# Kernel optimization log

Hardware: AMD Instinct MI355X
Metric: run time of the kernel (lower is better)

## Reference

```python
import jax, jax.numpy as jnp
import numpy as np

NUM_HEADS = 16


def setup_inputs() -> dict:
    key = jax.random.key(0)
    ks = jax.random.split(key, 6)
    B, N, L, C = 2, 1024, 4096, 1024
    x_obj = jax.random.normal(ks[0], (B, N, C), dtype=jnp.float32)
    x_ctx = jax.random.normal(ks[1], (B, L, C), dtype=jnp.float32)
    s = 1.0 / np.sqrt(C)
    Wq = jax.random.normal(ks[2], (C, C), dtype=jnp.float32) * s
    Wkv = jax.random.normal(ks[3], (C, 2 * C), dtype=jnp.float32) * s
    Wproj = jax.random.normal(ks[4], (C, C), dtype=jnp.float32) * s
    bproj = jax.random.normal(ks[5], (C,), dtype=jnp.float32) * 0.01
    return {"x_obj": x_obj, "x_ctx": x_ctx, "Wq": Wq, "Wkv": Wkv,
            "Wproj": Wproj, "bproj": bproj}


def _split_heads(t, H):
    # [B, T, C] -> [B, H, T, d]
    B, T, C = t.shape
    return t.reshape(B, T, H, C // H).transpose(0, 2, 1, 3)


def reference(x_obj, x_ctx, Wq, Wkv, Wproj, bproj):
    B, N, C = x_obj.shape
    H = NUM_HEADS
    d = C // H
    scale = d ** -0.5

    q = _split_heads(x_obj @ Wq, H)                      # [B,H,N,d]

    kv_o = x_obj @ Wkv                                   # [B,N,2C] -> (2,H,d) split
    k_obj = _split_heads(kv_o[..., :C], H)               # [B,H,N,d]
    v_obj = _split_heads(kv_o[..., C:], H)

    kv_c = x_ctx @ Wkv                                   # [B,L,2C]
    k_ctx = _split_heads(kv_c[..., :C], H)               # [B,H,L,d]
    v_ctx = _split_heads(kv_c[..., C:], H)

    k = jnp.concatenate([k_obj, k_ctx], axis=2)          # [B,H,N+L,d]
    v = jnp.concatenate([v_obj, v_ctx], axis=2)

    attn = jnp.einsum('bhnd,bhmd->bhnm', q, k) * scale   # [B,H,N,N+L]
    attn = jax.nn.softmax(attn, axis=-1)
    out = jnp.einsum('bhnm,bhmd->bhnd', attn, v)         # [B,H,N,d]
    out = out.transpose(0, 2, 1, 3).reshape(B, N, C)
    return out @ Wproj + bproj
```

## Files before the change

kernel.cpp:

```cpp
#include <hip/hip_runtime.h>
#include <stdint.h>

typedef unsigned short u16;
typedef unsigned int   u32;
typedef __attribute__((ext_vector_type(8))) short bf16x8;
typedef __attribute__((ext_vector_type(4))) float f32x4;

__device__ __forceinline__ u16 f2bf(float f) {
    union { float f; u32 u; } v; v.f = f;
    return (u16)((v.u + 0x7FFFu + ((v.u >> 16) & 1u)) >> 16);
}
__device__ __forceinline__ float bf2f(u16 h) {
    union { u32 u; float f; } v; v.u = ((u32)h) << 16; return v.f;
}
__device__ __forceinline__ u32 fbits(float f) {
    union { float f; u32 u; } v; v.f = f; return v.u;
}

__device__ __forceinline__ void async16(const u16* g, u16* l) {
    typedef __attribute__((address_space(1))) const u32 gq;
    typedef __attribute__((address_space(3))) u32 lq;
    __builtin_amdgcn_global_load_lds((gq*)g, (lq*)l, 16, 0, 0);
}

__global__ void cvt_all_k(const float* __restrict__ xo, const float* __restrict__ xc,
                          u16* __restrict__ Xc,
                          const float* __restrict__ Wq, const float* __restrict__ Wkv,
                          const float* __restrict__ Wp,
                          u16* __restrict__ Wqt, u16* __restrict__ Wkt,
                          u16* __restrict__ Wpt)
{
    __shared__ __align__(16) u16 Ts[64][72];
    int id = blockIdx.x, t = threadIdx.x;
    if (id < 10240) {
        int row = id, cid = t * 4;
        int b = row >= 5120, s = row - b * 5120;
        const float* src = (s < 1024)
            ? xo + ((size_t)(b * 1024 + s)) * 1024 + cid
            : xc + ((size_t)(b * 4096 + s - 1024)) * 1024 + cid;
        float4 f = *(const float4*)src;
        union { u16 a[4]; uint2 v; } p;
        p.a[0]=f2bf(f.x); p.a[1]=f2bf(f.y); p.a[2]=f2bf(f.z); p.a[3]=f2bf(f.w);
        *(uint2*)(Xc + (size_t)row * 1024 + cid) = p.v;
        return;
    }
    int wid = id - 10240;
    const float* W; u16* Wt; int N, tile;
    if (wid < 256)      { W = Wq;  Wt = Wqt; N = 1024; tile = wid; }
    else if (wid < 768) { W = Wkv; Wt = Wkt; N = 2048; tile = wid - 256; }
    else                { W = Wp;  Wt = Wpt; N = 1024; tile = wid - 768; }
    int nt = N >> 6;
    int n0 = (tile % nt) * 64, k0 = (tile / nt) * 64;
    int lr = t >> 2, lc = (t & 3) * 16;
    const float* src = W + (size_t)(k0 + lr) * N + n0 + lc;
    union { u16 a[8]; uint4 v; } p0, p1;
    float4 f0 = *(const float4*)(src),      f1 = *(const float4*)(src + 4);
    float4 f2 = *(const float4*)(src + 8),  f3 = *(const float4*)(src + 12);
    p0.a[0]=f2bf(f0.x); p0.a[1]=f2bf(f0.y); p0.a[2]=f2bf(f0.z); p0.a[3]=f2bf(f0.w);
    p0.a[4]=f2bf(f1.x); p0.a[5]=f2bf(f1.y); p0.a[6]=f2bf(f1.z); p0.a[7]=f2bf(f1.w);
    p1.a[0]=f2bf(f2.x); p1.a[1]=f2bf(f2.y); p1.a[2]=f2bf(f2.z); p1.a[3]=f2bf(f2.w);
    p1.a[4]=f2bf(f3.x); p1.a[5]=f2bf(f3.y); p1.a[6]=f2bf(f3.z); p1.a[7]=f2bf(f3.w);
    *(uint4*)&Ts[lr][lc]     = p0.v;
    *(uint4*)&Ts[lr][lc + 8] = p1.v;
    __syncthreads();
    union { u16 a[8]; uint4 v; } q0, q1;
#pragma unroll
    for (int j = 0; j < 8; ++j) q0.a[j] = Ts[lc + j][lr];
#pragma unroll
    for (int j = 0; j < 8; ++j) q1.a[j] = Ts[lc + 8 + j][lr];
    u16* dst = Wt + (size_t)(n0 + lr) * 1024 + k0 + lc;
    *(uint4*)dst       = q0.v;
    *(uint4*)(dst + 8) = q1.v;
}

__global__ __launch_bounds__(256, 2)
void gemm_qkv(const u16* __restrict__ A, const u16* __restrict__ Wqt,
              const u16* __restrict__ Wkt, u16* __restrict__ q,
              u16* __restrict__ Kh, u16* __restrict__ Vh)
{
    __shared__ __align__(16) u16 smem[17408];
    u16* As = smem;
    u16* Bs = smem + 4096;

    const int t = threadIdx.x, w = t >> 6;
    const int lane = t & 63, quad = lane >> 4, l16 = lane & 15;
    const int id = blockIdx.x;
    const bool qm = id >= 1280;
    int m0, n0; const u16* Bt;
    if (qm) { int t2 = id - 1280; m0 = (t2 >> 3) * 128; n0 = (t2 & 7) * 128; Bt = Wqt; }
    else    { m0 = (id >> 4) * 128; n0 = (id & 15) * 128; Bt = Wkt; }
    const int wr = (w >> 1) * 64, wc = (w & 1) * 64;

    const int sr0 = w * 32 + (lane >> 2), sr1 = sr0 + 16;
    const int cg  = (lane & 3) ^ ((lane >> 4) & 3);
    u16* abase = As + w * 1024;
    u16* bbase = Bs + w * 1024;

    const u16 *ar0, *ar1;
    {
        int g0 = m0 + sr0, g1 = m0 + sr1;
        if (qm) {
            ar0 = A + ((size_t)(g0 >> 10) * 5120 + (g0 & 1023)) * 1024;
            ar1 = A + ((size_t)(g1 >> 10) * 5120 + (g1 & 1023)) * 1024;
        } else {
            ar0 = A + (size_t)g0 * 1024;
            ar1 = A + (size_t)g1 * 1024;
        }
        ar0 += cg * 8; ar1 += cg * 8;
    }
    const u16* br0 = Bt + (size_t)(n0 + sr0) * 1024 + cg * 8;
    const u16* br1 = Bt + (size_t)(n0 + sr1) * 1024 + cg * 8;

    f32x4 acc[4][4] = {};
    const int sel = (quad ^ (l16 >> 2)) * 8;

    for (int k0 = 0; k0 < 1024; k0 += 32) {
        async16(ar0 + k0, abase);
        async16(ar1 + k0, abase + 512);
        async16(br0 + k0, bbase);
        async16(br1 + k0, bbase + 512);
        __syncthreads();

        bf16x8 av[4], bv[4];
#pragma unroll
        for (int i = 0; i < 4; ++i)
            av[i] = *(const bf16x8*)&As[(wr + i * 16 + l16) * 32 + sel];
#pragma unroll
        for (int j = 0; j < 4; ++j)
            bv[j] = *(const bf16x8*)&Bs[(wc + j * 16 + l16) * 32 + sel];
#pragma unroll
        for (int i = 0; i < 4; ++i)
#pragma unroll
            for (int j = 0; j < 4; ++j)
                acc[i][j] = __builtin_amdgcn_mfma_f32_16x16x32_bf16(av[i], bv[j], acc[i][j], 0, 0, 0);
        __syncthreads();
    }

    if (qm) {
        const float SC = 0.180336880f;
#pragma unroll
        for (int j = 0; j < 4; ++j) {
            int col = n0 + wc + j * 16 + l16;
#pragma unroll
            for (int i = 0; i < 4; ++i) {
                int rowb = m0 + wr + i * 16 + quad * 4;
#pragma unroll
                for (int r = 0; r < 4; ++r)
                    q[(size_t)(rowb + r) * 1024 + col] = f2bf(acc[i][j][r] * SC);
            }
        }
        return;
    }
    int b = m0 >= 5120;
    int keyb = m0 - b * 5120;
    if (n0 < 1024) {
#pragma unroll
        for (int j = 0; j < 4; ++j) {
            int col = n0 + wc + j * 16 + l16;
#pragma unroll
            for (int i = 0; i < 4; ++i) {
                int rowb = m0 + wr + i * 16 + quad * 4;
                int key = rowb - b * 5120;
                int bh = b * 16 + (col >> 6), d = col & 63;
                u16* dst = Kh + ((size_t)bh * 5120 + key) * 64 + d;
#pragma unroll
                for (int r = 0; r < 4; ++r) dst[r * 64] = f2bf(acc[i][j][r]);
            }
        }
    } else {
        u16* T = smem;
#pragma unroll
        for (int j = 0; j < 4; ++j) {
            int d2 = wc + j * 16 + l16;
#pragma unroll
            for (int i = 0; i < 4; ++i) {
                int kl = wr + i * 16 + quad * 4;
                union { u16 a[4]; uint2 v; } pk;
#pragma unroll
                for (int r = 0; r < 4; ++r) pk.a[r] = f2bf(acc[i][j][r]);
                *(uint2*)&T[d2 * 136 + kl] = pk.v;
            }
        }
        __syncthreads();
        int hb = (n0 - 1024) >> 6;
#pragma unroll
        for (int p = 0; p < 8; ++p) {
            int idx = p * 256 + t;
            int d2 = idx >> 4, k0c = (idx & 15) * 8;
            uint4 vv = *(const uint4*)&T[d2 * 136 + k0c];
            int bh = b * 16 + hb + (d2 >> 6), d = d2 & 63;
            *(uint4*)(Vh + ((size_t)bh * 64 + d) * 5120 + keyb + k0c) = vv;
        }
    }
}

__global__ __launch_bounds__(256, 2)
void gemm_proj(const u16* __restrict__ A, const u16* __restrict__ Bt,
               const float* __restrict__ bias, float* __restrict__ Cf)
{
    __shared__ __align__(16) u16 As[128 * 32];
    __shared__ __align__(16) u16 Bs[64 * 32];

    const int t = threadIdx.x, w = t >> 6;
    const int lane = t & 63, quad = lane >> 4, l16 = lane & 15;
    const int m0 = blockIdx.y * 128, n0 = blockIdx.x * 64;
    const int wr = w * 32;

    const int sr0 = w * 32 + (lane >> 2), sr1 = sr0 + 16;
    const int cg  = (lane & 3) ^ ((lane >> 4) & 3);
    u16* abase = As + w * 1024;
    u16* bbase = Bs + w * 512;

    const u16* ar0 = A + (size_t)(m0 + sr0) * 1024 + cg * 8;
    const u16* ar1 = A + (size_t)(m0 + sr1) * 1024 + cg * 8;
    const u16* br0 = Bt + (size_t)(n0 + w * 16 + (lane >> 2)) * 1024 + cg * 8;

    f32x4 acc[2][4] = {};
    const int sel = (quad ^ (l16 >> 2)) * 8;

    for (int k0 = 0; k0 < 1024; k0 += 32) {
        async16(ar0 + k0, abase);
        async16(ar1 + k0, abase + 512);
        async16(br0 + k0, bbase);
        __syncthreads();

        bf16x8 av[2], bv[4];
#pragma unroll
        for (int i = 0; i < 2; ++i)
            av[i] = *(const bf16x8*)&As[(wr + i * 16 + l16) * 32 + sel];
#pragma unroll
        for (int j = 0; j < 4; ++j)
            bv[j] = *(const bf16x8*)&Bs[(j * 16 + l16) * 32 + sel];
#pragma unroll
        for (int i = 0; i < 2; ++i)
#pragma unroll
            for (int j = 0; j < 4; ++j)
                acc[i][j] = __builtin_amdgcn_mfma_f32_16x16x32_bf16(av[i], bv[j], acc[i][j], 0, 0, 0);
        __syncthreads();
    }

#pragma unroll
    for (int j = 0; j < 4; ++j) {
        int col = n0 + j * 16 + l16;
        float bvl = bias[col];
#pragma unroll
        for (int i = 0; i < 2; ++i) {
            int rowb = m0 + wr + i * 16 + quad * 4;
#pragma unroll
            for (int r = 0; r < 4; ++r)
                Cf[(size_t)(rowb + r) * 1024 + col] = acc[i][j][r] + bvl;
        }
    }
}

__global__ __launch_bounds__(256, 4)
void attn_k(const u16* __restrict__ Q, const u16* __restrict__ Kh,
            const u16* __restrict__ Vh, u16* __restrict__ Op,
            float* __restrict__ Lp)
{
    __shared__ __align__(16) u16 Ks[4096];
    __shared__ __align__(16) u16 Vt[4096];
    __shared__ __align__(16) u16 Ps[8192];

    const int tid  = threadIdx.x;
    const int wave = tid >> 6, lane = tid & 63;
    const int quad = lane >> 4, l16 = lane & 15;
    const int bx = blockIdx.x;
    const int part = bx & 3, qt = (bx >> 2) & 7, h = (bx >> 5) & 15, b = bx >> 9;
    const int bh = b * 16 + h;

    const int qrow0 = b * 1024 + qt * 128 + wave * 32;
    const u16* qbase = Q + (size_t)qrow0 * 1024 + h * 64;

    bf16x8 aq[2][2];
#pragma unroll
    for (int rt = 0; rt < 2; ++rt) {
        aq[rt][0] = *(const bf16x8*)(qbase + (size_t)(rt * 16 + l16) * 1024 +      quad * 8);
        aq[rt][1] = *(const bf16x8*)(qbase + (size_t)(rt * 16 + l16) * 1024 + 32 + quad * 8);
    }

    union { u32 u[4]; bf16x8 v; } onesf;
#pragma unroll
    for (int i = 0; i < 4; ++i) onesf.u[i] = 0x3F803F80u;

    f32x4 o[2][4] = {};
    f32x4 lacc[2] = {};

    const u16* kbase = Kh + (size_t)bh * 5120 * 64;
    const u16* vbase = Vh + (size_t)bh * 64 * 5120;
    const int srow = tid >> 2;
    const int scg  = (tid & 3) * 2;
    const int m7   = srow & 7;
    const int l7   = l16 & 7;
    u16* kdst0 = Ks + srow * 64 + ((scg ^ m7) * 8);
    u16* kdst1 = Ks + srow * 64 + (((scg + 1) ^ m7) * 8);
    u16* vdst0 = Vt + srow * 64 + ((scg ^ m7) * 8);
    u16* vdst1 = Vt + srow * 64 + (((scg + 1) ^ m7) * 8);
    u16* psw   = Ps + wave * 2048;
    const int m_beg = part * 1280;

    for (int c = 0; c < 20; ++c) {
        const int m0 = m_beg + c * 64;
        {
            const u16* ks = kbase + (size_t)(m0 + srow) * 64 + scg * 8;
            *(uint4*)kdst0 = *(const uint4*)(ks);
            *(uint4*)kdst1 = *(const uint4*)(ks + 8);
        }
        {
            const u16* vs = vbase + (size_t)srow * 5120 + m0 + (tid & 3) * 4;
            uint2 g0 = *(const uint2*)(vs);
            uint2 g1 = *(const uint2*)(vs + 16);
            uint2 g2 = *(const uint2*)(vs + 32);
            uint2 g3 = *(const uint2*)(vs + 48);
            uint4 o0, o1;
            o0.x = __builtin_amdgcn_perm(g1.x, g0.x, 0x05040100u);
            o0.y = __builtin_amdgcn_perm(g3.x, g2.x, 0x05040100u);
            o0.z = __builtin_amdgcn_perm(g1.x, g0.x, 0x07060302u);
            o0.w = __builtin_amdgcn_perm(g3.x, g2.x, 0x07060302u);
            o1.x = __builtin_amdgcn_perm(g1.y, g0.y, 0x05040100u);
            o1.y = __builtin_amdgcn_perm(g3.y, g2.y, 0x05040100u);
            o1.z = __builtin_amdgcn_perm(g1.y, g0.y, 0x07060302u);
            o1.w = __builtin_amdgcn_perm(g3.y, g2.y, 0x07060302u);
            *(uint4*)vdst0 = o0;
            *(uint4*)vdst1 = o1;
        }
        __syncthreads();

        f32x4 s[2][4] = {};
#pragma unroll
        for (int nt = 0; nt < 4; ++nt) {
            const u16* krow = Ks + (nt * 16 + l16) * 64;
            bf16x8 kb0 = *(const bf16x8*)(krow + ((quad     ^ l7) * 8));
            bf16x8 kb1 = *(const bf16x8*)(krow + (((4+quad) ^ l7) * 8));
#pragma unroll
            for (int rt = 0; rt < 2; ++rt) {
                s[rt][nt] = __builtin_amdgcn_mfma_f32_16x16x32_bf16(aq[rt][0], kb0, s[rt][nt], 0, 0, 0);
                s[rt][nt] = __builtin_amdgcn_mfma_f32_16x16x32_bf16(aq[rt][1], kb1, s[rt][nt], 0, 0, 0);
            }
        }

#pragma unroll
        for (int rt = 0; rt < 2; ++rt)
#pragma unroll
            for (int r = 0; r < 4; ++r) {
                float e0 = exp2f(s[rt][0][r]);
                float e1 = exp2f(s[rt][1][r]);
                float e2 = exp2f(s[rt][2][r]);
                float e3 = exp2f(s[rt][3][r]);
                uint2 pw;
                pw.x = __builtin_amdgcn_perm(fbits(e1), fbits(e0), 0x07060302u);
                pw.y = __builtin_amdgcn_perm(fbits(e3), fbits(e2), 0x07060302u);
                int qr = quad * 4 + r;
                *(uint2*)(psw + (rt * 16 + qr) * 64 +
                          (((l16 >> 1) ^ (qr & 7)) * 8) + (l16 & 1) * 4) = pw;
            }

        asm volatile("s_waitcnt lgkmcnt(0)" ::: "memory");

        bf16x8 pf[2][2];
#pragma unroll
        for (int rt = 0; rt < 2; ++rt) {
            const u16* prow = psw + (rt * 16 + l16) * 64;
            pf[rt][0] = *(const bf16x8*)(prow + ((quad     ^ l7) * 8));
            pf[rt][1] = *(const bf16x8*)(prow + (((4+quad) ^ l7) * 8));
        }

#pragma unroll
        for (int rt = 0; rt < 2; ++rt) {
            lacc[rt] = __builtin_amdgcn_mfma_f32_16x16x32_bf16(pf[rt][0], onesf.v, lacc[rt], 0, 0, 0);
            lacc[rt] = __builtin_amdgcn_mfma_f32_16x16x32_bf16(pf[rt][1], onesf.v, lacc[rt], 0, 0, 0);
        }

#pragma unroll
        for (int dt = 0; dt < 4; ++dt) {
            const u16* vrow = Vt + (dt * 16 + l16) * 64;
            bf16x8 v0 = *(const bf16x8*)(vrow + ((quad     ^ l7) * 8));
            bf16x8 v1 = *(const bf16x8*)(vrow + (((4+quad) ^ l7) * 8));
#pragma unroll
            for (int rt = 0; rt < 2; ++rt) {
                o[rt][dt] = __builtin_amdgcn_mfma_f32_16x16x32_bf16(pf[rt][0], v0, o[rt][dt], 0, 0, 0);
                o[rt][dt] = __builtin_amdgcn_mfma_f32_16x16x32_bf16(pf[rt][1], v1, o[rt][dt], 0, 0, 0);
            }
        }
        __syncthreads();
    }

    const int Rb = bh * 1024 + qt * 128 + wave * 32;
    u16* obase = Op + ((size_t)part << 21);
#pragma unroll
    for (int rt = 0; rt < 2; ++rt)
#pragma unroll
        for (int dt = 0; dt < 4; ++dt)
#pragma unroll
            for (int r = 0; r < 4; ++r) {
                int R = Rb + rt * 16 + quad * 4 + r;
                obase[(size_t)R * 64 + dt * 16 + l16] = f2bf(o[rt][dt][r]);
            }
    if (l16 == 0) {
#pragma unroll
        for (int rt = 0; rt < 2; ++rt)
#pragma unroll
            for (int r = 0; r < 4; ++r)
                Lp[part * 32768 + Rb + rt * 16 + quad * 4 + r] = lacc[rt][r];
    }
}

__global__ void comb_k(const u16* __restrict__ Op, const float* __restrict__ Lp,
                       u16* __restrict__ ao)
{
    int t = blockIdx.x * 256 + threadIdx.x;
    int R = t >> 4, dg = (t & 15) * 4;
    float l = Lp[R] + Lp[32768 + R] + Lp[65536 + R] + Lp[98304 + R];
    float a[4] = {0.f, 0.f, 0.f, 0.f};
#pragma unroll
    for (int p = 0; p < 4; ++p) {
        union { u16 a[4]; uint2 v; } w;
        w.v = *(const uint2*)(Op + ((size_t)p << 21) + (size_t)R * 64 + dg);
#pragma unroll
        for (int j = 0; j < 4; ++j) a[j] += bf2f(w.a[j]);
    }
    float inv = 1.f / l;
    int bh = R >> 10, n = R & 1023, b = bh >> 4, h = bh & 15;
    union { u16 a[4]; uint2 v; } out;
#pragma unroll
    for (int j = 0; j < 4; ++j) out.a[j] = f2bf(a[j] * inv);
    *(uint2*)(ao + (size_t)(b * 1024 + n) * 1024 + h * 64 + dg) = out.v;
}

extern "C" void kernel_launch(void* const* d_in, const int* in_sizes, int n_in,
                              void* d_out, int out_size, void* d_ws, size_t ws_size,
                              hipStream_t stream)
{
    const float* x_obj = (const float*)d_in[0];
    const float* x_ctx = (const float*)d_in[1];
    const float* Wq    = (const float*)d_in[2];
    const float* Wkv   = (const float*)d_in[3];
    const float* Wproj = (const float*)d_in[4];
    const float* bproj = (const float*)d_in[5];
    float* out = (float*)d_out;

    u16* Xc  = (u16*)d_ws;
    u16* ao  = Xc;
    u16* Op  = Xc + (size_t)2097152;
    u16* Wqt = Xc  + (size_t)10485760;
    u16* Wkt = Wqt + (size_t)1048576;
    u16* Wpt = Wkt + (size_t)2097152;
    u16* q   = Wpt + (size_t)1048576;
    u16* Kh  = q   + (size_t)2097152;
    u16* Vh  = Kh  + (size_t)10485760;
    float* Lp = (float*)(Vh + (size_t)10485760);

    dim3 blk(256);
    cvt_all_k<<<dim3(11264), blk, 0, stream>>>(x_obj, x_ctx, Xc,
                                               Wq, Wkv, Wproj, Wqt, Wkt, Wpt);
    gemm_qkv<<<dim3(1408), blk, 0, stream>>>(Xc, Wqt, Wkt, q, Kh, Vh);
    attn_k<<<dim3(1024), blk, 0, stream>>>(q, Kh, Vh, Op, Lp);
    comb_k<<<dim3(2048), blk, 0, stream>>>(Op, Lp, ao);
    gemm_proj<<<dim3(16, 16), blk, 0, stream>>>(ao, Wpt, bproj, out);
}
```

Before: 252.1 us.

## Use async global-to-LDS loads in attention and split KV into five parts

Measured after the change: 419.0 us. 66.2% more time.

```diff
diff --git a/kernel.cpp b/kernel.cpp
--- a/kernel.cpp
+++ b/kernel.cpp
@@ -253,7 +253,7 @@
     }
 }
 
-__global__ __launch_bounds__(256, 4)
+__global__ __launch_bounds__(256, 5)
 void attn_k(const u16* __restrict__ Q, const u16* __restrict__ Kh,
             const u16* __restrict__ Vh, u16* __restrict__ Op,
             float* __restrict__ Lp)
@@ -266,7 +266,8 @@
     const int wave = tid >> 6, lane = tid & 63;
     const int quad = lane >> 4, l16 = lane & 15;
     const int bx = blockIdx.x;
-    const int part = bx & 3, qt = (bx >> 2) & 7, h = (bx >> 5) & 15, b = bx >> 9;
+    const int part = blockIdx.y;
+    const int qt = bx & 7, h = (bx >> 3) & 15, b = bx >> 7;
     const int bh = b * 16 + h;
 
     const int qrow0 = b * 1024 + qt * 128 + wave * 32;
@@ -288,42 +289,22 @@
 
     const u16* kbase = Kh + (size_t)bh * 5120 * 64;
     const u16* vbase = Vh + (size_t)bh * 64 * 5120;
-    const int srow = tid >> 2;
-    const int scg  = (tid & 3) * 2;
-    const int m7   = srow & 7;
-    const int l7   = l16 & 7;
-    u16* kdst0 = Ks + srow * 64 + ((scg ^ m7) * 8);
-    u16* kdst1 = Ks + srow * 64 + (((scg + 1) ^ m7) * 8);
-    u16* vdst0 = Vt + srow * 64 + ((scg ^ m7) * 8);
-    u16* vdst1 = Vt + srow * 64 + (((scg + 1) ^ m7) * 8);
+    const int arow = lane >> 3, achk = lane & 7;
+    const int axor = (achk ^ arow) * 8;
+    const u16* kst = kbase + (size_t)(wave * 16 + arow) * 64 + axor;
+    const u16* vst = vbase + (size_t)(wave * 16 + arow) * 5120 + axor;
+    u16* klds0 = Ks + wave * 1024;
+    u16* vlds0 = Vt + wave * 1024;
     u16* psw   = Ps + wave * 2048;
-    const int m_beg = part * 1280;
-
-    for (int c = 0; c < 20; ++c) {
+    const int l7 = l16 & 7;
+    const int m_beg = part * 1024;
+
+    for (int c = 0; c < 16; ++c) {
         const int m0 = m_beg + c * 64;
-        {
-            const u16* ks = kbase + (size_t)(m0 + srow) * 64 + scg * 8;
-            *(uint4*)kdst0 = *(const uint4*)(ks);
-            *(uint4*)kdst1 = *(const uint4*)(ks + 8);
-        }
-        {
-            const u16* vs = vbase + (size_t)srow * 5120 + m0 + (tid & 3) * 4;
-            uint2 g0 = *(const uint2*)(vs);
-            uint2 g1 = *(const uint2*)(vs + 16);
-            uint2 g2 = *(const uint2*)(vs + 32);
-            uint2 g3 = *(const uint2*)(vs + 48);
-            uint4 o0, o1;
-            o0.x = __builtin_amdgcn_perm(g1.x, g0.x, 0x05040100u);
-            o0.y = __builtin_amdgcn_perm(g3.x, g2.x, 0x05040100u);
-            o0.z = __builtin_amdgcn_perm(g1.x, g0.x, 0x07060302u);
-            o0.w = __builtin_amdgcn_perm(g3.x, g2.x, 0x07060302u);
-            o1.x = __builtin_amdgcn_perm(g1.y, g0.y, 0x05040100u);
-            o1.y = __builtin_amdgcn_perm(g3.y, g2.y, 0x05040100u);
-            o1.z = __builtin_amdgcn_perm(g1.y, g0.y, 0x07060302u);
-            o1.w = __builtin_amdgcn_perm(g3.y, g2.y, 0x07060302u);
-            *(uint4*)vdst0 = o0;
-            *(uint4*)vdst1 = o1;
-        }
+        async16(kst + (size_t)m0 * 64,       klds0);
+        async16(kst + (size_t)m0 * 64 + 512, klds0 + 512);
+        async16(vst + m0,                    vlds0);
+        async16(vst + m0 + (size_t)8 * 5120, vlds0 + 512);
         __syncthreads();
 
         f32x4 s[2][4] = {};
@@ -343,16 +324,14 @@
         for (int rt = 0; rt < 2; ++rt)
 #pragma unroll
             for (int r = 0; r < 4; ++r) {
-                float e0 = exp2f(s[rt][0][r]);
-                float e1 = exp2f(s[rt][1][r]);
-                float e2 = exp2f(s[rt][2][r]);
-                float e3 = exp2f(s[rt][3][r]);
-                uint2 pw;
-                pw.x = __builtin_amdgcn_perm(fbits(e1), fbits(e0), 0x07060302u);
-                pw.y = __builtin_amdgcn_perm(fbits(e3), fbits(e2), 0x07060302u);
                 int qr = quad * 4 + r;
-                *(uint2*)(psw + (rt * 16 + qr) * 64 +
-                          (((l16 >> 1) ^ (qr & 7)) * 8) + (l16 & 1) * 4) = pw;
+                u16* pr = psw + (rt * 16 + qr) * 64;
+#pragma unroll
+                for (int nt = 0; nt < 4; ++nt) {
+                    float e = exp2f(s[rt][nt][r]);
+                    pr[(((nt * 2 + (l16 >> 3)) ^ (qr & 7)) * 8) + l7] =
+                        (u16)(fbits(e) >> 16);
+                }
             }
 
         asm volatile("s_waitcnt lgkmcnt(0)" ::: "memory");
@@ -410,10 +389,12 @@
 {
     int t = blockIdx.x * 256 + threadIdx.x;
     int R = t >> 4, dg = (t & 15) * 4;
-    float l = Lp[R] + Lp[32768 + R] + Lp[65536 + R] + Lp[98304 + R];
+    float l = 0.f;
+#pragma unroll
+    for (int p = 0; p < 5; ++p) l += Lp[p * 32768 + R];
     float a[4] = {0.f, 0.f, 0.f, 0.f};
 #pragma unroll
-    for (int p = 0; p < 4; ++p) {
+    for (int p = 0; p < 5; ++p) {
         union { u16 a[4]; uint2 v; } w;
         w.v = *(const uint2*)(Op + ((size_t)p << 21) + (size_t)R * 64 + dg);
 #pragma unroll
@@ -440,10 +421,10 @@
     float* out = (float*)d_out;
 
     u16* Xc  = (u16*)d_ws;
-    u16* ao  = Xc;
-    u16* Op  = Xc + (size_t)2097152;
+    u16* Op  = Xc;
     u16* Wqt = Xc  + (size_t)10485760;
     u16* Wkt = Wqt + (size_t)1048576;
+    u16* ao  = Wkt;
     u16* Wpt = Wkt + (size_t)2097152;
     u16* q   = Wpt + (size_t)1048576;
     u16* Kh  = q   + (size_t)2097152;
@@ -454,7 +435,7 @@
     cvt_all_k<<<dim3(11264), blk, 0, stream>>>(x_obj, x_ctx, Xc,
                                                Wq, Wkv, Wproj, Wqt, Wkt, Wpt);
     gemm_qkv<<<dim3(1408), blk, 0, stream>>>(Xc, Wqt, Wkt, q, Kh, Vh);
-    attn_k<<<dim3(1024), blk, 0, stream>>>(q, Kh, Vh, Op, Lp);
+    attn_k<<<dim3(256, 5), blk, 0, stream>>>(q, Kh, Vh, Op, Lp);
     comb_k<<<dim3(2048), blk, 0, stream>>>(Op, Lp, ao);
     gemm_proj<<<dim3(16, 16), blk, 0, stream>>>(ao, Wpt, bproj, out);
 }
```
